# Kernel optimization log

Hardware: AMD Instinct MI355X
Metric: run time of the kernel (lower is better)

Reference implementation:

```python
import jax, jax.numpy as jnp
import numpy as np
from jax import lax

# Resolved Optuna hyperparameters
NPOINTS = (512, 256, 128)
RADII = (0.2, 0.4, 0.8)
KS = (32, 32, 32)
BN_EPS = 1e-5


def _fps_single(pts, npoint):
    """Farthest point sampling on one cloud. pts: (N,3) -> (npoint,) int32."""
    N = pts.shape[0]
    def step(carry, _):
        dists, last = carry
        d = jnp.sum((pts - pts[last]) ** 2, axis=-1)
        dists = jnp.minimum(dists, d)
        nxt = jnp.argmax(dists).astype(jnp.int32)
        return (dists, nxt), last
    init = (jnp.full((N,), 1e10, pts.dtype), jnp.int32(0))
    (_, _), idx = lax.scan(step, init, None, length=npoint)
    return idx


def _set_abstraction(xyz, feat, W, b, radius, k, npoint):
    """xyz: (B,N,3), feat: (B,N,C_in) -> new_xyz (B,S,3), new_feat (B,S,C_out)."""
    B, N, _ = xyz.shape
    fps_idx = jax.vmap(lambda p: _fps_single(p, npoint))(xyz)          # (B,S)
    new_xyz = jax.vmap(lambda x, i: x[i])(xyz, fps_idx)                # (B,S,3)
    # ball query: squared distances centers -> all points
    d2 = jnp.sum((new_xyz[:, :, None, :] - xyz[:, None, :, :]) ** 2, axis=-1)  # (B,S,N)
    valid = d2 <= radius * radius
    ar = jnp.arange(N, dtype=jnp.int32)
    gi = jnp.where(valid, ar[None, None, :], N)                        # invalid -> N
    gi = jnp.sort(gi, axis=-1)[:, :, :k]                               # first k in index order
    first = gi[:, :, :1]
    gi = jnp.where(gi == N, first, gi)                                 # pad with first valid (center itself)
    g_xyz = jax.vmap(lambda x, i: x[i])(xyz, gi)                       # (B,S,k,3)
    rel = g_xyz - new_xyz[:, :, None, :]
    g_feat = jax.vmap(lambda x, i: x[i])(feat, gi)                     # (B,S,k,C_in)
    h = jnp.concatenate([rel, g_feat], axis=-1)                        # (B,S,k,3+C_in)
    h = jax.nn.relu(jnp.einsum('bskc,co->bsko', h, W) + b)
    return new_xyz, jnp.max(h, axis=2)                                 # max-pool over group


def _bn(x, g, b):
    # nn.BatchNorm1d training-mode forward (batch statistics, biased var)
    m = x.mean(axis=0)
    v = x.var(axis=0)
    return (x - m) * lax.rsqrt(v + BN_EPS) * g + b


def setup_inputs() -> dict:
    key = jax.random.key(0)
    ks = jax.random.split(key, 8)
    def w(k, i, o):
        return (jax.random.normal(k, (i, o), jnp.float32) / np.sqrt(i)).astype(jnp.float32)
    return dict(
        points=jax.random.uniform(ks[0], (16, 4096, 3), jnp.float32),
        W1=w(ks[1], 3 + 3, 64),   b1=jnp.zeros((64,), jnp.float32),
        W2=w(ks[2], 64 + 3, 128), b2=jnp.zeros((128,), jnp.float32),
        W3=w(ks[3], 128 + 3, 256), b3=jnp.zeros((256,), jnp.float32),
        fc1_w=w(ks[4], 256, 256), fc1_b=jnp.zeros((256,), jnp.float32),
        fc2_w=w(ks[5], 256, 128), fc2_b=jnp.zeros((128,), jnp.float32),
        fc3_w=w(ks[6], 128, 12),  fc3_b=jnp.zeros((12,), jnp.float32),
        bn1_g=jnp.ones((256,), jnp.float32), bn1_b=jnp.zeros((256,), jnp.float32),
        bn2_g=jnp.ones((128,), jnp.float32), bn2_b=jnp.zeros((128,), jnp.float32),
    )


def reference(points, W1, b1, W2, b2, W3, b3, fc1_w, fc1_b, fc2_w, fc2_b,
              fc3_w, fc3_b, bn1_g, bn1_b, bn2_g, bn2_b):
    B = points.shape[0]
    xyz, feat = points, points
    for (W, bb, r, k, s) in ((W1, b1, RADII[0], KS[0], NPOINTS[0]),
                             (W2, b2, RADII[1], KS[1], NPOINTS[1]),
                             (W3, b3, RADII[2], KS[2], NPOINTS[2])):
        xyz, feat = _set_abstraction(xyz, feat, W, bb, r, k, s)
    f = jnp.max(feat, axis=1)                                          # (B, ch3)
    x = jax.nn.relu(_bn(f @ fc1_w + fc1_b, bn1_g, bn1_b))              # dropout: eval-mode identity
    x = jax.nn.relu(_bn(x @ fc2_w + fc2_b, bn2_g, bn2_b))
    x = x @ fc3_w + fc3_b
    return x.reshape(B, 4, 3)
```

## Files before the change

kernel.cpp:

```cpp
#include <hip/hip_runtime.h>
#include <hip/hip_bf16.h>


#define B_SZ 16

template<int CTRL>
__device__ __forceinline__ float dpp_mv(float v) {
    const int i = __float_as_int(v);
    const int r = __builtin_amdgcn_update_dpp(i, i, CTRL, 0xf, 0xf, false);
    return __int_as_float(r);
}

__device__ __forceinline__ float wave_max_f32(float x) {
    float v = x;
    v = fmaxf(v, dpp_mv<0x111>(v));
    v = fmaxf(v, dpp_mv<0x112>(v));
    v = fmaxf(v, dpp_mv<0x114>(v));
    v = fmaxf(v, dpp_mv<0x118>(v));
    v = fmaxf(v, dpp_mv<0x142>(v));
    v = fmaxf(v, dpp_mv<0x143>(v));
    return __uint_as_float(__builtin_amdgcn_readlane(__float_as_uint(v), 63));
}

__device__ __forceinline__ float read_lane_f32(float v, int l) {
    return __uint_as_float(__builtin_amdgcn_readlane(__float_as_uint(v), l));
}

template<int N, int NPOINT, int BLOCK, int S0, int S1, bool FIRST>
__device__ __forceinline__ void fps_body(
    const float* __restrict__ xyz,
    float* __restrict__ newxyz,
    float* __restrict__ dstate,
    const int b)
{
    constexpr int P  = N / BLOCK;
    constexpr int NW = BLOCK / 64;
    constexpr int O0 = FIRST ? 0 : S0;
    __shared__ float4 part[2][NW];
    __shared__ float  outb[(S1 - O0) * 3];

    const int tid = threadIdx.x;
    const int lane = tid & 63, w = tid >> 6;
    const float* xb = xyz + (size_t)b * N * 3;

    float px[P], py[P], pz[P], dd[P];
    const int base = tid * P;
#pragma unroll
    for (int i = 0; i < P; i++) {
        px[i] = xb[(base + i) * 3 + 0];
        py[i] = xb[(base + i) * 3 + 1];
        pz[i] = xb[(base + i) * 3 + 2];
    }
    float lx, ly, lz;
    if (FIRST) {
#pragma unroll
        for (int i = 0; i < P; i++) dd[i] = 1e10f;
        lx = xb[0]; ly = xb[1]; lz = xb[2];
        if (tid == 0) { outb[0] = lx; outb[1] = ly; outb[2] = lz; }
    } else {
#pragma unroll
        for (int i = 0; i < P; i++) dd[i] = dstate[((size_t)b * P + i) * BLOCK + tid];
        const float* c = newxyz + ((size_t)b * NPOINT + (S0 - 1)) * 3;
        lx = c[0]; ly = c[1]; lz = c[2];
    }

    for (int s = S0; s < S1; s++) {
        float bv = -1.0f, bx = 0.0f, by = 0.0f, bz = 0.0f;
#pragma unroll
        for (int i = 0; i < P; i++) {
            const float dx = px[i] - lx, dy = py[i] - ly, dz = pz[i] - lz;
            const float d2 = __fadd_rn(__fadd_rn(__fmul_rn(dx, dx), __fmul_rn(dy, dy)),
                                       __fmul_rn(dz, dz));
            const float nd = fminf(dd[i], d2);
            dd[i] = nd;
            const bool gt = nd > bv;
            bv = gt ? nd : bv;
            bx = gt ? px[i] : bx;
            by = gt ? py[i] : by;
            bz = gt ? pz[i] : bz;
        }
        const float wmax = wave_max_f32(bv);
        const unsigned long long mset = __ballot(bv == wmax);
        const int li = __ffsll(mset) - 1;
        const int buf = s & 1;
        if (lane == li) part[buf][w] = make_float4(bv, bx, by, bz);
        __syncthreads();
        float cv = -1.0f;
#pragma unroll
        for (int q = 0; q < NW; q++) {
            const float4 pq = part[buf][q];
            const bool gt = pq.x > cv;
            cv = gt ? pq.x : cv;
            lx = gt ? pq.y : lx;
            ly = gt ? pq.z : ly;
            lz = gt ? pq.w : lz;
        }
        if (tid == 0) {
            const int t = (s - O0) * 3;
            outb[t + 0] = lx; outb[t + 1] = ly; outb[t + 2] = lz;
        }
    }
    __syncthreads();
    if (S1 < NPOINT) {
#pragma unroll
        for (int i = 0; i < P; i++)
            dstate[((size_t)b * P + i) * BLOCK + tid] = dd[i];
    }
    float* o = newxyz + ((size_t)b * NPOINT + O0) * 3;
    for (int t = tid; t < (S1 - O0) * 3; t += BLOCK) o[t] = outb[t];
}

template<int N, int NPOINT, int BLOCK, int S0, int S1, bool FIRST>
__global__ __launch_bounds__(BLOCK) void fps_kernel(
    const float* __restrict__ xyz, float* __restrict__ newxyz,
    float* __restrict__ dstate)
{
    fps_body<N, NPOINT, BLOCK, S0, S1, FIRST>(xyz, newxyz, dstate, blockIdx.x);
}

template<int N, int NPOINT>
__device__ __forceinline__ void fps_wave_body(
    const float* __restrict__ xyz,
    float* __restrict__ newxyz,
    const int b, const int lane)
{
    constexpr int P = N / 64;
    const float* xb = xyz + (size_t)b * N * 3;

    float px[P], py[P], pz[P], dd[P];
    const int base = lane * P;
#pragma unroll
    for (int i = 0; i < P; i++) {
        px[i] = xb[(base + i) * 3 + 0];
        py[i] = xb[(base + i) * 3 + 1];
        pz[i] = xb[(base + i) * 3 + 2];
        dd[i] = 1e10f;
    }
#pragma unroll
    for (int i = 0; i < P; i++) {
        asm volatile("" : "+v"(px[i]), "+v"(py[i]), "+v"(pz[i]));
    }
    float lx = xb[0], ly = xb[1], lz = xb[2];
    if (lane == 0) {
        float* o = newxyz + (size_t)b * NPOINT * 3;
        o[0] = lx; o[1] = ly; o[2] = lz;
    }

    for (int s = 1; s < NPOINT; s++) {
        float bv = -1.0f, bx = 0.0f, by = 0.0f, bz = 0.0f;
#pragma unroll
        for (int i = 0; i < P; i++) {
            const float dx = px[i] - lx, dy = py[i] - ly, dz = pz[i] - lz;
            const float d2 = __fadd_rn(__fadd_rn(__fmul_rn(dx, dx), __fmul_rn(dy, dy)),
                                       __fmul_rn(dz, dz));
            const float nd = fminf(dd[i], d2);
            dd[i] = nd;
            const bool gt = nd > bv;
            bv = gt ? nd : bv;
            bx = gt ? px[i] : bx;
            by = gt ? py[i] : by;
            bz = gt ? pz[i] : bz;
        }
        const float wmax = wave_max_f32(bv);
        const unsigned long long mset = __ballot(bv == wmax);
        const int li = __ffsll(mset) - 1;
        lx = read_lane_f32(bx, li);
        ly = read_lane_f32(by, li);
        lz = read_lane_f32(bz, li);
        if (lane == 0) {
            float* o = newxyz + ((size_t)b * NPOINT + s) * 3;
            o[0] = lx; o[1] = ly; o[2] = lz;
        }
    }
}

template<int N, int S, int CF, int COUT, int R, bool AMAX>
__device__ __forceinline__ void sa_body(
    const float* __restrict__ xyz,
    const float* __restrict__ feat,
    const float* __restrict__ cent,
    const float* __restrict__ W,
    const float* __restrict__ bias,
    float* __restrict__ outf,
    const float r2, const int s, const int b, const int lane,
    const int obase, int* __restrict__ gi, float* __restrict__ h)
{
    constexpr int K    = 32;
    constexpr int JT   = 16;
    constexpr int CIN  = CF + 3;
    constexpr int CINP = (CIN + 3) & ~3;
    constexpr int C4   = CIN & ~3;

    const float* xb = xyz  + (size_t)b * N * 3;
    const float* fb = feat + (size_t)b * N * CF;
    const float cx = cent[((size_t)b * S + s) * 3 + 0];
    const float cy = cent[((size_t)b * S + s) * 3 + 1];
    const float cz = cent[((size_t)b * S + s) * 3 + 2];

    constexpr int RND = N / 256;
    int total = 0, g0 = 0;
    for (int r0 = 0; r0 < RND; r0++) {
        if (total >= K) break;
        float xs[4], ys[4], zs[4];
#pragma unroll
        for (int c4 = 0; c4 < 4; c4++) {
            const int p = (r0 * 4 + c4) * 64 + lane;
            xs[c4] = xb[p * 3 + 0];
            ys[c4] = xb[p * 3 + 1];
            zs[c4] = xb[p * 3 + 2];
        }
#pragma unroll
        for (int c4 = 0; c4 < 4; c4++) {
            const int p = (r0 * 4 + c4) * 64 + lane;
            const float dx = xs[c4] - cx, dy = ys[c4] - cy, dz = zs[c4] - cz;
            const float d2 = __fadd_rn(__fadd_rn(__fmul_rn(dx, dx), __fmul_rn(dy, dy)),
                                       __fmul_rn(dz, dz));
            const bool v = (d2 <= r2);
            const unsigned long long bal = __ballot(v);
            if (total == 0 && bal != 0ull) g0 = (r0 * 4 + c4) * 64 + (__ffsll(bal) - 1);
            const int pos = total + __popcll(bal & ((1ull << lane) - 1ull));
            if (v && pos < K) gi[pos] = p;
            total += __popcll(bal);
        }
    }
    if (lane == 0 && total < K) {
        for (int q = total; q < K; q++) gi[q] = g0;
    }
    __syncthreads();

    float m[R];
#pragma unroll
    for (int r = 0; r < R; r++) m[r] = -1e30f;

    for (int pass = 0; pass < K / JT; pass++) {
        for (int jj = 0; jj < JT; jj++) {
            const int idx = gi[pass * JT + jj];
            for (int c = lane; c < CIN; c += 64) {
                float val;
                if (c < 3) {
                    const float cc = (c == 0) ? cx : ((c == 1) ? cy : cz);
                    val = xb[idx * 3 + c] - cc;
                } else {
                    val = fb[(size_t)idx * CF + (c - 3)];
                }
                h[jj * CINP + c] = val;
            }
        }
        __syncthreads();

        float acc[JT][R];
#pragma unroll
        for (int jj = 0; jj < JT; jj++)
#pragma unroll
            for (int r = 0; r < R; r++) acc[jj][r] = 0.0f;

        const float* wp = W + obase + lane;
        int c = 0;
        for (; c < C4; c += 4) {
            float wv[4][R];
#pragma unroll
            for (int q = 0; q < 4; q++)
#pragma unroll
                for (int r = 0; r < R; r++)
                    wv[q][r] = wp[(size_t)(c + q) * COUT + r * 64];
#pragma unroll
            for (int jj = 0; jj < JT; jj++) {
                const float4 hv = *(const float4*)&h[jj * CINP + c];
#pragma unroll
                for (int r = 0; r < R; r++) {
                    acc[jj][r] = fmaf(hv.x, wv[0][r], acc[jj][r]);
                    acc[jj][r] = fmaf(hv.y, wv[1][r], acc[jj][r]);
                    acc[jj][r] = fmaf(hv.z, wv[2][r], acc[jj][r]);
                    acc[jj][r] = fmaf(hv.w, wv[3][r], acc[jj][r]);
                }
            }
        }
        for (; c < CIN; c++) {
            float wv[R];
#pragma unroll
            for (int r = 0; r < R; r++) wv[r] = wp[(size_t)c * COUT + r * 64];
#pragma unroll
            for (int jj = 0; jj < JT; jj++) {
                const float hv = h[jj * CINP + c];
#pragma unroll
                for (int r = 0; r < R; r++)
                    acc[jj][r] = fmaf(hv, wv[r], acc[jj][r]);
            }
        }
#pragma unroll
        for (int jj = 0; jj < JT; jj++)
#pragma unroll
            for (int r = 0; r < R; r++) m[r] = fmaxf(m[r], acc[jj][r]);
        __syncthreads();
    }

#pragma unroll
    for (int r = 0; r < R; r++) {
        const int o = obase + r * 64 + lane;
        const float val = fmaxf(bias[o] + m[r], 0.0f);
        if (AMAX) {
            atomicMax((unsigned*)&outf[(size_t)b * COUT + o], __float_as_uint(val));
        } else {
            outf[((size_t)b * S + s) * COUT + o] = val;
        }
    }
}

template<int N, int S, int CF, int COUT, int R, int HALVES, bool AMAX>
__global__ __launch_bounds__(64) void sa_kernel(
    const float* __restrict__ xyz, const float* __restrict__ feat,
    const float* __restrict__ cent, const float* __restrict__ W,
    const float* __restrict__ bias, float* __restrict__ outf, const float r2)
{
    constexpr int CINP = (CF + 3 + 3) & ~3;
    __shared__ int   gi[32];
    __shared__ float h[16 * CINP];
    const int s = blockIdx.x / HALVES;
    const int obase = (blockIdx.x % HALVES) * R * 64;
    sa_body<N, S, CF, COUT, R, AMAX>(xyz, feat, cent, W, bias, outf, r2,
                                     s, blockIdx.y, threadIdx.x, obase, gi, h);
}

template<int S0, int S1, int SOFF, int SCNT>
__global__ __launch_bounds__(512) void fused_fps1_sa_kernel(
    const float* __restrict__ fxyz, float* __restrict__ fnew,
    float* __restrict__ fdd,
    const float* __restrict__ xyz, const float* __restrict__ feat,
    const float* __restrict__ cent, const float* __restrict__ W,
    const float* __restrict__ bias, float* __restrict__ outf, const float r2)
{
    constexpr int CINP = 8;
    if (blockIdx.x < B_SZ) {
        __builtin_amdgcn_s_setprio(3);
        fps_body<4096, 512, 512, S0, S1, false>(fxyz, fnew, fdd, blockIdx.x);
    } else {
        __shared__ int   gi_s[8][32];
        __shared__ float h_s[8][16 * CINP];
        const int w = threadIdx.x >> 6, lane = threadIdx.x & 63;
        const int widx = (blockIdx.x - B_SZ) * 8 + w;
        const int b = widx / SCNT, s = SOFF + widx % SCNT;
        sa_body<4096, 512, 3, 64, 1, false>(xyz, feat, cent, W, bias, outf, r2,
                                            s, b, lane, 0, gi_s[w], h_s[w]);
    }
}

template<int NF, int NPF, int N, int S, int CF, int COUT, int R,
         int SOFF, int SCNT, int HALVES, bool ZERO>
__global__ __launch_bounds__(64) void fused_fps_sa_kernel(
    const float* __restrict__ fxyz,
    float* __restrict__ fnew,
    const float* __restrict__ xyz, const float* __restrict__ feat,
    const float* __restrict__ cent, const float* __restrict__ W,
    const float* __restrict__ bias, float* __restrict__ outf,
    float* __restrict__ fmx, const float r2)
{
    constexpr int CINP = (CF + 3 + 3) & ~3;
    if (blockIdx.x < B_SZ) {
        if (ZERO) {
            ((float4*)fmx)[blockIdx.x * 64 + threadIdx.x] =
                make_float4(0.f, 0.f, 0.f, 0.f);
        }
        __builtin_amdgcn_s_setprio(3);
        fps_wave_body<NF, NPF>(fxyz, fnew, blockIdx.x, threadIdx.x);
    } else {
        __shared__ int   gi[32];
        __shared__ float h[16 * CINP];
        const int i = blockIdx.x - B_SZ;
        const int obase = (i % HALVES) * R * 64;
        const int j = i / HALVES;
        sa_body<N, S, CF, COUT, R, false>(xyz, feat, cent, W, bias, outf, r2,
                                          SOFF + j % SCNT, j / SCNT,
                                          threadIdx.x, obase, gi, h);
    }
}

__global__ __launch_bounds__(64) void fc1_kernel(
    const float* __restrict__ f,
    const float* __restrict__ w,
    const float* __restrict__ bias,
    float* __restrict__ x1h)
{
    const int r = blockIdx.x >> 2;
    const int o = (blockIdx.x & 3) * 64 + threadIdx.x;
    const float* fr = f + r * 256;
    float acc = bias[o];
    for (int c = 0; c < 256; c += 4) {
        acc = fmaf(fr[c + 0], w[(size_t)(c + 0) * 256 + o], acc);
        acc = fmaf(fr[c + 1], w[(size_t)(c + 1) * 256 + o], acc);
        acc = fmaf(fr[c + 2], w[(size_t)(c + 2) * 256 + o], acc);
        acc = fmaf(fr[c + 3], w[(size_t)(c + 3) * 256 + o], acc);
    }
    x1h[r * 256 + o] = acc;
}

__global__ __launch_bounds__(256) void head2_kernel(
    const float* __restrict__ x1h,
    const float* __restrict__ fc2_w, const float* __restrict__ fc2_b,
    const float* __restrict__ fc3_w, const float* __restrict__ fc3_b,
    const float* __restrict__ bn1_g, const float* __restrict__ bn1_b,
    const float* __restrict__ bn2_g, const float* __restrict__ bn2_b,
    float* __restrict__ out)
{
    __shared__ float x1[16 * 257];
    __shared__ float x2[16 * 129];
    const int tid = threadIdx.x;

    for (int idx = tid; idx < 16 * 256; idx += 256) {
        const int r = idx >> 8, c = idx & 255;
        x1[r * 257 + c] = x1h[idx];
    }
    __syncthreads();
    {
        const int o = tid;
        float v[16];
#pragma unroll
        for (int r = 0; r < 16; r++) v[r] = x1[r * 257 + o];
        float m = 0.0f;
#pragma unroll
        for (int r = 0; r < 16; r++) m += v[r];
        m *= (1.0f / 16.0f);
        float var = 0.0f;
#pragma unroll
        for (int r = 0; r < 16; r++) { const float d = v[r] - m; var += d * d; }
        var *= (1.0f / 16.0f);
        const float sc = bn1_g[o] / sqrtf(var + 1e-5f);
        const float sh = bn1_b[o];
#pragma unroll
        for (int r = 0; r < 16; r++)
            x1[r * 257 + o] = fmaxf((v[r] - m) * sc + sh, 0.0f);
    }
    __syncthreads();
    {
        const int r = tid >> 4, g = tid & 15;
        float acc[8];
#pragma unroll
        for (int i = 0; i < 8; i++) acc[i] = fc2_b[g * 8 + i];
        const float* wrow = fc2_w + g * 8;
        for (int c = 0; c < 256; c++) {
            const float fv = x1[r * 257 + c];
            const float4* w4 = (const float4*)(wrow + (size_t)c * 128);
#pragma unroll
            for (int q = 0; q < 2; q++) {
                const float4 wv = w4[q];
                acc[q * 4 + 0] = fmaf(fv, wv.x, acc[q * 4 + 0]);
                acc[q * 4 + 1] = fmaf(fv, wv.y, acc[q * 4 + 1]);
                acc[q * 4 + 2] = fmaf(fv, wv.z, acc[q * 4 + 2]);
                acc[q * 4 + 3] = fmaf(fv, wv.w, acc[q * 4 + 3]);
            }
        }
#pragma unroll
        for (int i = 0; i < 8; i++) x2[r * 129 + g * 8 + i] = acc[i];
    }
    __syncthreads();
    if (tid < 128) {
        const int o = tid;
        float v[16];
#pragma unroll
        for (int r = 0; r < 16; r++) v[r] = x2[r * 129 + o];
        float m = 0.0f;
#pragma unroll
        for (int r = 0; r < 16; r++) m += v[r];
        m *= (1.0f / 16.0f);
        float var = 0.0f;
#pragma unroll
        for (int r = 0; r < 16; r++) { const float d = v[r] - m; var += d * d; }
        var *= (1.0f / 16.0f);
        const float sc = bn2_g[o] / sqrtf(var + 1e-5f);
        const float sh = bn2_b[o];
#pragma unroll
        for (int r = 0; r < 16; r++)
            x2[r * 129 + o] = fmaxf((v[r] - m) * sc + sh, 0.0f);
    }
    __syncthreads();
    if (tid < 192) {
        const int r = tid / 12, j = tid - r * 12;
        float acc = fc3_b[j];
        for (int c = 0; c < 128; c++)
            acc = fmaf(x2[r * 129 + c], fc3_w[c * 12 + j], acc);
        out[r * 12 + j] = acc;
    }
}

extern "C" void kernel_launch(void* const* d_in, const int* in_sizes, int n_in,
                              void* d_out, int out_size, void* d_ws, size_t ws_size,
                              hipStream_t stream) {
    const float* points = (const float*)d_in[0];
    const float* W1     = (const float*)d_in[1];
    const float* b1     = (const float*)d_in[2];
    const float* W2     = (const float*)d_in[3];
    const float* b2     = (const float*)d_in[4];
    const float* W3     = (const float*)d_in[5];
    const float* b3     = (const float*)d_in[6];
    const float* fc1_w  = (const float*)d_in[7];
    const float* fc1_b  = (const float*)d_in[8];
    const float* fc2_w  = (const float*)d_in[9];
    const float* fc2_b  = (const float*)d_in[10];
    const float* fc3_w  = (const float*)d_in[11];
    const float* fc3_b  = (const float*)d_in[12];
    const float* bn1_g  = (const float*)d_in[13];
    const float* bn1_b  = (const float*)d_in[14];
    const float* bn2_g  = (const float*)d_in[15];
    const float* bn2_b  = (const float*)d_in[16];
    float* out = (float*)d_out;

    float* ws   = (float*)d_ws;
    float* nx1  = ws;
    float* f1   = nx1 + 24576;
    float* nx2  = f1  + 524288;
    float* f2   = nx2 + 12288;
    float* nx3  = f2  + 524288;
    float* fmx  = nx3 + 6144;
    float* fdd  = fmx + 4096;
    float* x1h  = fdd + 65536;

    const float r21 = (float)(0.2 * 0.2);
    fps_kernel<4096, 512, 512, 1, 128, true><<<B_SZ, 512, 0, stream>>>(
        points, nx1, fdd);
    fused_fps1_sa_kernel<128, 256, 0, 128><<<B_SZ + 256, 512, 0, stream>>>(
        points, nx1, fdd, points, points, nx1, W1, b1, f1, r21);
    fused_fps1_sa_kernel<256, 384, 128, 128><<<B_SZ + 256, 512, 0, stream>>>(
        points, nx1, fdd, points, points, nx1, W1, b1, f1, r21);
    fused_fps1_sa_kernel<384, 512, 256, 128><<<B_SZ + 256, 512, 0, stream>>>(
        points, nx1, fdd, points, points, nx1, W1, b1, f1, r21);
    fused_fps_sa_kernel<512, 256, 4096, 512, 3, 64, 1, 384, 128, 1, true>
        <<<B_SZ + 128 * B_SZ, 64, 0, stream>>>(
        nx1, nx2, points, points, nx1, W1, b1, f1, fmx, r21);
    fused_fps_sa_kernel<256, 128, 512, 256, 64, 128, 1, 0, 256, 2, false>
        <<<B_SZ + 2 * 256 * B_SZ, 64, 0, stream>>>(
        nx2, nx3, nx1, f1, nx2, W2, b2, f2, fmx, (float)(0.4 * 0.4));
    sa_kernel<256, 128, 128, 256, 2, 2, true>
        <<<dim3(128 * 2, B_SZ), 64, 0, stream>>>(
        nx2, f2, nx3, W3, b3, fmx, (float)(0.8 * 0.8));
    fc1_kernel<<<64, 64, 0, stream>>>(fmx, fc1_w, fc1_b, x1h);
    head2_kernel<<<1, 256, 0, stream>>>(x1h, fc2_w, fc2_b, fc3_w, fc3_b,
                                        bn1_g, bn1_b, bn2_g, bn2_b, out);
}
```

Before: 719.2 us.

## Split stage-2/3 FPS into segments overlapped with SA of prior centers

The single-wave FPS for the second and third set-abstraction levels now runs in segments that save their min-distance state to workspace and resume later. Each segment runs in the same launch as SA work on centers that are already known. This lets SA2 run on its first 128 centers while FPS2 finishes, and SA3 run on its first 64 centers while FPS3 finishes, hiding the serial FPS latency. The cost is extra launches, state save and restore traffic, and new workspace buffers.

```diff
diff --git a/kernel.cpp b/kernel.cpp
--- a/kernel.cpp
+++ b/kernel.cpp
@@ -118,10 +118,11 @@
     fps_body<N, NPOINT, BLOCK, S0, S1, FIRST>(xyz, newxyz, dstate, blockIdx.x);
 }
 
-template<int N, int NPOINT>
-__device__ __forceinline__ void fps_wave_body(
+template<int N, int NPOINT, int S0, int S1, bool FIRST>
+__device__ __forceinline__ void fps_wave_seg_body(
     const float* __restrict__ xyz,
     float* __restrict__ newxyz,
+    float* __restrict__ dstate,
     const int b, const int lane)
 {
     constexpr int P = N / 64;
@@ -134,19 +135,28 @@
         px[i] = xb[(base + i) * 3 + 0];
         py[i] = xb[(base + i) * 3 + 1];
         pz[i] = xb[(base + i) * 3 + 2];
-        dd[i] = 1e10f;
     }
 #pragma unroll
     for (int i = 0; i < P; i++) {
         asm volatile("" : "+v"(px[i]), "+v"(py[i]), "+v"(pz[i]));
     }
-    float lx = xb[0], ly = xb[1], lz = xb[2];
-    if (lane == 0) {
-        float* o = newxyz + (size_t)b * NPOINT * 3;
-        o[0] = lx; o[1] = ly; o[2] = lz;
-    }
-
-    for (int s = 1; s < NPOINT; s++) {
+    float lx, ly, lz;
+    if (FIRST) {
+#pragma unroll
+        for (int i = 0; i < P; i++) dd[i] = 1e10f;
+        lx = xb[0]; ly = xb[1]; lz = xb[2];
+        if (lane == 0) {
+            float* o = newxyz + (size_t)b * NPOINT * 3;
+            o[0] = lx; o[1] = ly; o[2] = lz;
+        }
+    } else {
+#pragma unroll
+        for (int i = 0; i < P; i++) dd[i] = dstate[(size_t)b * N + i * 64 + lane];
+        const float* c = newxyz + ((size_t)b * NPOINT + (S0 - 1)) * 3;
+        lx = c[0]; ly = c[1]; lz = c[2];
+    }
+
+    for (int s = S0; s < S1; s++) {
         float bv = -1.0f, bx = 0.0f, by = 0.0f, bz = 0.0f;
 #pragma unroll
         for (int i = 0; i < P; i++) {
@@ -171,6 +181,11 @@
             float* o = newxyz + ((size_t)b * NPOINT + s) * 3;
             o[0] = lx; o[1] = ly; o[2] = lz;
         }
+    }
+    if (S1 < NPOINT) {
+#pragma unroll
+        for (int i = 0; i < P; i++)
+            dstate[(size_t)b * N + i * 64 + lane] = dd[i];
     }
 }
 
@@ -306,7 +321,7 @@
     }
 }
 
-template<int N, int S, int CF, int COUT, int R, int HALVES, bool AMAX>
+template<int N, int S, int CF, int COUT, int R, int SOFF, int HALVES, bool AMAX>
 __global__ __launch_bounds__(64) void sa_kernel(
     const float* __restrict__ xyz, const float* __restrict__ feat,
     const float* __restrict__ cent, const float* __restrict__ W,
@@ -315,7 +330,7 @@
     constexpr int CINP = (CF + 3 + 3) & ~3;
     __shared__ int   gi[32];
     __shared__ float h[16 * CINP];
-    const int s = blockIdx.x / HALVES;
+    const int s = SOFF + blockIdx.x / HALVES;
     const int obase = (blockIdx.x % HALVES) * R * 64;
     sa_body<N, S, CF, COUT, R, AMAX>(xyz, feat, cent, W, bias, outf, r2,
                                      s, blockIdx.y, threadIdx.x, obase, gi, h);
@@ -344,11 +359,13 @@
     }
 }
 
-template<int NF, int NPF, int N, int S, int CF, int COUT, int R,
-         int SOFF, int SCNT, int HALVES, bool ZERO>
-__global__ __launch_bounds__(64) void fused_fps_sa_kernel(
+template<int NF, int NPF, int FS0, int FS1, bool FFIRST,
+         int N, int S, int CF, int COUT, int R,
+         int SOFF, int SCNT, int HALVES, bool AMAX, bool ZERO>
+__global__ __launch_bounds__(64) void fused_fpsw_sa_kernel(
     const float* __restrict__ fxyz,
     float* __restrict__ fnew,
+    float* __restrict__ fdst,
     const float* __restrict__ xyz, const float* __restrict__ feat,
     const float* __restrict__ cent, const float* __restrict__ W,
     const float* __restrict__ bias, float* __restrict__ outf,
@@ -361,16 +378,17 @@
                 make_float4(0.f, 0.f, 0.f, 0.f);
         }
         __builtin_amdgcn_s_setprio(3);
-        fps_wave_body<NF, NPF>(fxyz, fnew, blockIdx.x, threadIdx.x);
+        fps_wave_seg_body<NF, NPF, FS0, FS1, FFIRST>(fxyz, fnew, fdst,
+                                                     blockIdx.x, threadIdx.x);
     } else {
         __shared__ int   gi[32];
         __shared__ float h[16 * CINP];
         const int i = blockIdx.x - B_SZ;
         const int obase = (i % HALVES) * R * 64;
         const int j = i / HALVES;
-        sa_body<N, S, CF, COUT, R, false>(xyz, feat, cent, W, bias, outf, r2,
-                                          SOFF + j % SCNT, j / SCNT,
-                                          threadIdx.x, obase, gi, h);
+        sa_body<N, S, CF, COUT, R, AMAX>(xyz, feat, cent, W, bias, outf, r2,
+                                         SOFF + j % SCNT, j / SCNT,
+                                         threadIdx.x, obase, gi, h);
     }
 }
 
@@ -511,9 +529,14 @@
     float* nx3  = f2  + 524288;
     float* fmx  = nx3 + 6144;
     float* fdd  = fmx + 4096;
-    float* x1h  = fdd + 65536;
+    float* fdd2 = fdd + 65536;
+    float* fdd3 = fdd2 + 8192;
+    float* x1h  = fdd3 + 4096;
 
     const float r21 = (float)(0.2 * 0.2);
+    const float r22 = (float)(0.4 * 0.4);
+    const float r23 = (float)(0.8 * 0.8);
+
     fps_kernel<4096, 512, 512, 1, 128, true><<<B_SZ, 512, 0, stream>>>(
         points, nx1, fdd);
     fused_fps1_sa_kernel<128, 256, 0, 128><<<B_SZ + 256, 512, 0, stream>>>(
@@ -522,15 +545,25 @@
         points, nx1, fdd, points, points, nx1, W1, b1, f1, r21);
     fused_fps1_sa_kernel<384, 512, 256, 128><<<B_SZ + 256, 512, 0, stream>>>(
         points, nx1, fdd, points, points, nx1, W1, b1, f1, r21);
-    fused_fps_sa_kernel<512, 256, 4096, 512, 3, 64, 1, 384, 128, 1, true>
+    fused_fpsw_sa_kernel<512, 256, 1, 128, true,
+                         4096, 512, 3, 64, 1, 384, 128, 1, false, true>
         <<<B_SZ + 128 * B_SZ, 64, 0, stream>>>(
-        nx1, nx2, points, points, nx1, W1, b1, f1, fmx, r21);
-    fused_fps_sa_kernel<256, 128, 512, 256, 64, 128, 1, 0, 256, 2, false>
-        <<<B_SZ + 2 * 256 * B_SZ, 64, 0, stream>>>(
-        nx2, nx3, nx1, f1, nx2, W2, b2, f2, fmx, (float)(0.4 * 0.4));
-    sa_kernel<256, 128, 128, 256, 2, 2, true>
-        <<<dim3(128 * 2, B_SZ), 64, 0, stream>>>(
-        nx2, f2, nx3, W3, b3, fmx, (float)(0.8 * 0.8));
+        nx1, nx2, fdd2, points, points, nx1, W1, b1, f1, fmx, r21);
+    fused_fpsw_sa_kernel<512, 256, 128, 256, false,
+                         512, 256, 64, 128, 2, 0, 128, 1, false, false>
+        <<<B_SZ + 128 * B_SZ, 64, 0, stream>>>(
+        nx1, nx2, fdd2, nx1, f1, nx2, W2, b2, f2, fmx, r22);
+    fused_fpsw_sa_kernel<256, 128, 1, 64, true,
+                         512, 256, 64, 128, 2, 128, 128, 1, false, false>
+        <<<B_SZ + 128 * B_SZ, 64, 0, stream>>>(
+        nx2, nx3, fdd3, nx1, f1, nx2, W2, b2, f2, fmx, r22);
+    fused_fpsw_sa_kernel<256, 128, 64, 128, false,
+                         256, 128, 128, 256, 2, 0, 64, 2, true, false>
+        <<<B_SZ + 64 * 2 * B_SZ, 64, 0, stream>>>(
+        nx2, nx3, fdd3, nx2, f2, nx3, W3, b3, fmx, fmx, r23);
+    sa_kernel<256, 128, 128, 256, 2, 64, 2, true>
+        <<<dim3(64 * 2, B_SZ), 64, 0, stream>>>(
+        nx2, f2, nx3, W3, b3, fmx, r23);
     fc1_kernel<<<64, 64, 0, stream>>>(fmx, fc1_w, fc1_b, x1h);
     head2_kernel<<<1, 256, 0, stream>>>(x1h, fc2_w, fc2_b, fc3_w, fc3_b,
                                         bn1_g, bn1_b, bn2_g, bn2_b, out);
```

Result: slower. 790.0 us (+9.8%).
